# Kernel optimization log

Hardware: AMD Instinct MI355X
Metric: run time of the kernel (lower is better)

The kernel has to match this reference:

```python
import jax, jax.numpy as jnp
import numpy as np

E, H = 512, 256  # embed_dim, hidden_dim
B, SQ, SK = 2, 512, 512


def _linear_params(k, fin, fout):
    lim = 1.0 / np.sqrt(fin)
    kw, kb = jax.random.split(k)
    W = jax.random.uniform(kw, (fin, fout), minval=-lim, maxval=lim, dtype=jnp.float32)
    b = jax.random.uniform(kb, (fout,), minval=-lim, maxval=lim, dtype=jnp.float32)
    return W, b


def setup_inputs() -> dict:
    rng = jax.random.key(0)
    ks = jax.random.split(rng, 12)
    query = jax.random.normal(ks[0], (B, SQ, E), dtype=jnp.float32)
    key = jax.random.normal(ks[1], (B, SK, E), dtype=jnp.float32)
    Wqe, bqe = _linear_params(ks[2], E, H)
    Wke, bke = _linear_params(ks[3], E, H)
    W1, b1 = _linear_params(ks[4], 2 * H, H)  # importance_predictor layer 0
    W2, b2 = _linear_params(ks[5], H, H)      # layer 1
    W3, b3 = _linear_params(ks[6], H, H)      # layer 2
    Wf, bf = _linear_params(ks[7], H, 1)      # final importance logit
    Wv1, bv1 = _linear_params(ks[8], 2 * H, H)  # variance_estimator layer 0
    Wv2, bv2 = _linear_params(ks[9], H, 1)      # variance_estimator final
    return {"query": query, "key": key,
            "Wqe": Wqe, "bqe": bqe, "Wke": Wke, "bke": bke,
            "W1": W1, "b1": b1, "W2": W2, "b2": b2, "W3": W3, "b3": b3,
            "Wf": Wf, "bf": bf, "Wv1": Wv1, "bv1": bv1, "Wv2": Wv2, "bv2": bv2}


def reference(query, key, Wqe, bqe, Wke, bke, W1, b1, W2, b2, W3, b3, Wf, bf, Wv1, bv1, Wv2, bv2):
    # Encoders (dropout is identity at eval)
    qf = jax.nn.relu(jnp.einsum('bqe,eh->bqh', query, Wqe) + bqe)  # [B,Sq,H]
    kf = jax.nn.relu(jnp.einsum('bke,eh->bkh', key, Wke) + bke)    # [B,Sk,H]

    # First Linear(2H,H) on cat([q,k]) == q@W1[:H] + k@W1[H:]; broadcast over pairs
    qp = jnp.einsum('bqh,hd->bqd', qf, W1[:H])
    kp = jnp.einsum('bkh,hd->bkd', kf, W1[H:])
    h = jax.nn.relu(qp[:, :, None, :] + kp[:, None, :, :] + b1)  # [B,Sq,Sk,H]
    h = jax.nn.relu(jnp.einsum('bqkh,hd->bqkd', h, W2) + b2)
    h = jax.nn.relu(jnp.einsum('bqkh,hd->bqkd', h, W3) + b3)
    importance_logits = (jnp.einsum('bqkh,ho->bqko', h, Wf) + bf)[..., 0]  # [B,Sq,Sk]

    # Variance head: Linear(2H,H) split the same way, ReLU, Linear, Softplus
    vq = jnp.einsum('bqh,hd->bqd', qf, Wv1[:H])
    vk = jnp.einsum('bkh,hd->bkd', kf, Wv1[H:])
    v = jax.nn.relu(vq[:, :, None, :] + vk[:, None, :, :] + bv1)  # [B,Sq,Sk,H]
    estimated_variance = jax.nn.softplus((jnp.einsum('bqkh,ho->bqko', v, Wv2) + bv2)[..., 0])
    return importance_logits, estimated_variance
```

## Files before the change

kernel.cpp:

```cpp
#include <hip/hip_runtime.h>
#include <hip/hip_bf16.h>
#include <cstdint>
#include <cstddef>
#include <cstring>

#define HDIM 256
#define EDIM 512
#define NB   2
#define NSQ  512
#define NSK  512

typedef _Float16 f16x8 __attribute__((ext_vector_type(8)));
typedef _Float16 h2    __attribute__((ext_vector_type(2)));
typedef __fp16   fp16v2 __attribute__((ext_vector_type(2)));
typedef float    f32x4 __attribute__((ext_vector_type(4)));
typedef unsigned short u16x8 __attribute__((ext_vector_type(8)));

#define OFF_W2F  0u
#define OFF_W3F  65536u
#define OFF_WQEF 131072u
#define OFF_WKEF 262144u
#define OFF_WCQ  393216u
#define OFF_WCK  524288u
#define OFF_WV2H 655360u
#define F16_WS_END_BYTES 1312768u

union U8 { f16x8 v; h2 h[4]; };

__device__ __forceinline__ ushort2 f2h2(float x, float y) {
  fp16v2 r = __builtin_amdgcn_cvt_pkrtz(x, y);
  ushort2 u;
  __builtin_memcpy(&u, &r, 4);
  return u;
}
__device__ __forceinline__ float relu_(float x) { return x > 0.f ? x : 0.f; }
__device__ __forceinline__ float softplus_(float x) {
  return fmaxf(x, 0.f) + log1pf(expf(-fabsf(x)));
}

__global__ __launch_bounds__(64) void shuffle_weights(
    const float* __restrict__ Wqe, const float* __restrict__ Wke,
    const float* __restrict__ W1,  const float* __restrict__ Wv1,
    const float* __restrict__ W2,  const float* __restrict__ W3,
    const float* __restrict__ Wv2,
    unsigned short* __restrict__ wsb)
{
  const int bx = blockIdx.x;
  const int lane = threadIdx.x;
  if (bx == 1280) {
    float a = Wv2[lane * 4 + 0], b = Wv2[lane * 4 + 1];
    float c = Wv2[lane * 4 + 2], d = Wv2[lane * 4 + 3];
    ushort2 lo = f2h2(a, b), hi = f2h2(c, d);
    ushort4 o; o.x = lo.x; o.y = lo.y; o.z = hi.x; o.w = hi.y;
    *(ushort4*)&wsb[OFF_WV2H + lane * 4] = o;
    return;
  }
  const float* src; unsigned short* dst; int S; int idx;
  if      (bx <  128) { src = W2;          dst = wsb + OFF_W2F;           S = 8;  idx = bx;        }
  else if (bx <  256) { src = W3;          dst = wsb + OFF_W3F;           S = 8;  idx = bx - 128;  }
  else if (bx <  512) { src = Wqe;         dst = wsb + OFF_WQEF;          S = 16; idx = bx - 256;  }
  else if (bx <  768) { src = Wke;         dst = wsb + OFF_WKEF;          S = 16; idx = bx - 512;  }
  else if (bx <  896) { src = W1;          dst = wsb + OFF_WCQ;           S = 8;  idx = bx - 768;  }
  else if (bx < 1024) { src = Wv1;         dst = wsb + OFF_WCQ + 65536u;  S = 8;  idx = bx - 896;  }
  else if (bx < 1152) { src = W1 + 65536;  dst = wsb + OFF_WCK;           S = 8;  idx = bx - 1024; }
  else                { src = Wv1 + 65536; dst = wsb + OFF_WCK + 65536u;  S = 8;  idx = bx - 1152; }
  const int t = idx / S, s = idx % S;
  const int n  = t * 16 + (lane & 15);
  const int k0 = s * 32 + ((lane >> 4) << 3);
  unsigned short* o = dst + ((size_t)(t * S + s) * 64 + lane) * 8;
  #pragma unroll
  for (int j = 0; j < 8; j += 2) {
    ushort2 pp = f2h2(src[(size_t)(k0 + j) * 256 + n], src[(size_t)(k0 + j + 1) * 256 + n]);
    *(ushort2*)&o[j] = pp;
  }
}

__global__ __launch_bounds__(256) void encoder_kernel(
    const float* __restrict__ query, const float* __restrict__ key,
    const float* __restrict__ bqe,   const float* __restrict__ bke,
    const float* __restrict__ b1,    const float* __restrict__ bv1,
    const unsigned short* __restrict__ WqeF, const unsigned short* __restrict__ WkeF,
    const unsigned short* __restrict__ WcqF, const unsigned short* __restrict__ WckF,
    _Float16* __restrict__ Pq, _Float16* __restrict__ Pk)
{
  __shared__ unsigned short sX[32 * 520];
  __shared__ unsigned short sF[32 * 264];
  __shared__ float sBe[256];
  __shared__ float sBc[512];

  const int bx   = blockIdx.x;
  const int side = bx >> 5;
  const int rt   = bx & 31;
  const int t    = threadIdx.x;

  const float* Xsrc = side ? key : query;
  const unsigned short* WeF = side ? WkeF : WqeF;
  const unsigned short* WcF = side ? WckF : WcqF;
  _Float16* P = side ? Pk : Pq;

  {
    const int m = t >> 3, ch = t & 7;
    const int c0 = ch * 64;
    const float* xr = Xsrc + (size_t)(rt * 32 + m) * EDIM;
    #pragma unroll
    for (int cc = 0; cc < 64; cc += 4) {
      const int c = c0 + cc;
      float4 xv = *(const float4*)(xr + c);
      ushort2 lo = f2h2(xv.x, xv.y);
      ushort2 hi = f2h2(xv.z, xv.w);
      ushort4 xb; xb.x = lo.x; xb.y = lo.y; xb.z = hi.x; xb.w = hi.y;
      *(ushort4*)&sX[m * 520 + c] = xb;
    }
    sBe[t]       = side ? bke[t] : bqe[t];
    sBc[t]       = side ? 0.f : b1[t];
    sBc[256 + t] = side ? 0.f : bv1[t];
  }
  __syncthreads();

  const int wave = t >> 6, lane = t & 63;
  const int l15 = lane & 15, q4 = lane >> 4;

  f32x4 acc1[4][2];
  #pragma unroll
  for (int ft = 0; ft < 4; ++ft)
    #pragma unroll
    for (int pt = 0; pt < 2; ++pt)
      acc1[ft][pt] = (f32x4){0.f, 0.f, 0.f, 0.f};

  for (int s = 0; s < 16; ++s) {
    f16x8 af[4], bfr[2];
    #pragma unroll
    for (int ft = 0; ft < 4; ++ft) {
      const int tg = wave * 4 + ft;
      af[ft] = *(const f16x8*)(WeF + ((size_t)(tg * 16 + s) * 64 + lane) * 8);
    }
    #pragma unroll
    for (int pt = 0; pt < 2; ++pt)
      bfr[pt] = *(const f16x8*)&sX[(pt * 16 + l15) * 520 + s * 32 + q4 * 8];
    #pragma unroll
    for (int ft = 0; ft < 4; ++ft)
      #pragma unroll
      for (int pt = 0; pt < 2; ++pt)
        acc1[ft][pt] = __builtin_amdgcn_mfma_f32_16x16x32_f16(af[ft], bfr[pt], acc1[ft][pt], 0, 0, 0);
  }

  #pragma unroll
  for (int ft = 0; ft < 4; ++ft) {
    const int tg = wave * 4 + ft;
    const int n0 = tg * 16 + q4 * 4;
    float4 b4 = *(const float4*)&sBe[n0];
    #pragma unroll
    for (int pt = 0; pt < 2; ++pt) {
      const int mr = pt * 16 + l15;
      f32x4 a = acc1[ft][pt];
      ushort2 lo = f2h2(relu_(a[0] + b4.x), relu_(a[1] + b4.y));
      ushort2 hi = f2h2(relu_(a[2] + b4.z), relu_(a[3] + b4.w));
      ushort4 h; h.x = lo.x; h.y = lo.y; h.z = hi.x; h.w = hi.y;
      *(ushort4*)&sF[mr * 264 + n0] = h;
    }
  }
  __syncthreads();

  f32x4 acc2[8][2];
  #pragma unroll
  for (int ft = 0; ft < 8; ++ft)
    #pragma unroll
    for (int pt = 0; pt < 2; ++pt)
      acc2[ft][pt] = (f32x4){0.f, 0.f, 0.f, 0.f};

  for (int s = 0; s < 8; ++s) {
    f16x8 af[8], bfr[2];
    #pragma unroll
    for (int ft = 0; ft < 8; ++ft) {
      const int tg = wave * 8 + ft;
      af[ft] = *(const f16x8*)(WcF + ((size_t)(tg * 8 + s) * 64 + lane) * 8);
    }
    #pragma unroll
    for (int pt = 0; pt < 2; ++pt)
      bfr[pt] = *(const f16x8*)&sF[(pt * 16 + l15) * 264 + s * 32 + q4 * 8];
    #pragma unroll
    for (int ft = 0; ft < 8; ++ft)
      #pragma unroll
      for (int pt = 0; pt < 2; ++pt)
        acc2[ft][pt] = __builtin_amdgcn_mfma_f32_16x16x32_f16(af[ft], bfr[pt], acc2[ft][pt], 0, 0, 0);
  }

  #pragma unroll
  for (int ft = 0; ft < 8; ++ft) {
    const int tg = wave * 8 + ft;
    const int n0 = tg * 16 + q4 * 4;
    float4 bc = *(const float4*)&sBc[n0];
    #pragma unroll
    for (int pt = 0; pt < 2; ++pt) {
      const int mr = pt * 16 + l15;
      const int row = rt * 32 + mr;
      f32x4 a = acc2[ft][pt];
      ushort2 lo = f2h2(a[0] + bc.x, a[1] + bc.y);
      ushort2 hi = f2h2(a[2] + bc.z, a[3] + bc.w);
      ushort4 o; o.x = lo.x; o.y = lo.y; o.z = hi.x; o.w = hi.y;
      *(ushort4*)((unsigned short*)P + (size_t)row * 512 + n0) = o;
    }
  }
}

__global__ __launch_bounds__(512, 4) void pair_kernel(
    const _Float16* __restrict__ Pq, const _Float16* __restrict__ Pk,
    const unsigned short* __restrict__ W2F, const unsigned short* __restrict__ W3F,
    const float* __restrict__ b2, const float* __restrict__ b3,
    const float* __restrict__ Wf, const float* __restrict__ bfp,
    const unsigned short* __restrict__ Wv2H, const float* __restrict__ bv2p,
    float* __restrict__ out)
{
  __shared__ __align__(16) unsigned char smem[35840];
  unsigned short* sXH = (unsigned short*)smem;
  float* sB2   = (float*)(smem + 32768);
  float* sB3   = (float*)(smem + 33792);
  float* sWf   = (float*)(smem + 34816);
  float* sRed  = (float*)(smem + 32768);

  const int kt = blockIdx.x, qy = blockIdx.y, bz = blockIdx.z;
  const int t = threadIdx.x;
  const _Float16* qpRow = Pq + (size_t)(bz * NSQ + qy) * 512;

  const int wave = t >> 6, lane = t & 63;
  const int l15 = lane & 15, q4 = lane >> 4;
  const int lsw = l15 & 7;

  const unsigned short* a2base = W2F + ((size_t)(wave * 2) * 8 * 64 + lane) * 8;
  const unsigned short* a3base = W3F + ((size_t)(wave * 2) * 8 * 64 + lane) * 8;

  f16x8 afd[2][2];
  afd[0][0] = *(const f16x8*)(a2base);
  afd[0][1] = *(const f16x8*)(a2base + 8 * 64 * 8);

  {
    const int m   = t >> 3;
    const int sub = t & 7;
    const _Float16* kpRow = Pk + (size_t)(bz * NSK + kt * 64 + m) * 512;
    const int msw = (m & 7);
    const f16x8 z8 = {0, 0, 0, 0, 0, 0, 0, 0};
    float vpart = 0.f;
    #pragma unroll
    for (int it = 0; it < 4; ++it) {
      const int c = it * 64 + sub * 8;
      f16x8 q8 = *(const f16x8*)(qpRow + c);
      f16x8 k8 = *(const f16x8*)(kpRow + c);
      f16x8 r  = __builtin_elementwise_max(q8 + k8, z8);
      const int chunk = (c >> 3) ^ msw;
      *(f16x8*)&sXH[m * 256 + chunk * 8] = r;
      f16x8 a8 = *(const f16x8*)(qpRow + 256 + c);
      f16x8 v8 = *(const f16x8*)(kpRow + 256 + c);
      U8 ar; ar.v = __builtin_elementwise_max(a8 + v8, z8);
      U8 w8; w8.v = *(const f16x8*)((const _Float16*)Wv2H + c);
      vpart = __builtin_amdgcn_fdot2(ar.h[0], w8.h[0], vpart, false);
      vpart = __builtin_amdgcn_fdot2(ar.h[1], w8.h[1], vpart, false);
      vpart = __builtin_amdgcn_fdot2(ar.h[2], w8.h[2], vpart, false);
      vpart = __builtin_amdgcn_fdot2(ar.h[3], w8.h[3], vpart, false);
    }
    vpart += __shfl_xor(vpart, 1, 64);
    vpart += __shfl_xor(vpart, 2, 64);
    vpart += __shfl_xor(vpart, 4, 64);
    if (sub == 0) {
      const size_t o = (size_t)(bz * NSQ + qy) * NSK + kt * 64 + m;
      out[(size_t)NB * NSQ * NSK + o] = softplus_(vpart + bv2p[0]);
    }
    if (t < 256) { sB2[t] = b2[t]; sB3[t] = b3[t]; sWf[t] = Wf[t]; }
  }
  __syncthreads();

  f32x4 acc[2][4];
  #pragma unroll
  for (int ft = 0; ft < 2; ++ft)
    #pragma unroll
    for (int pt = 0; pt < 4; ++pt)
      acc[ft][pt] = (f32x4){0.f, 0.f, 0.f, 0.f};

  #pragma unroll
  for (int s = 0; s < 8; ++s) {
    if (s < 7) {
      afd[(s + 1) & 1][0] = *(const f16x8*)(a2base + (size_t)(s + 1) * 512);
      afd[(s + 1) & 1][1] = *(const f16x8*)(a2base + 8 * 64 * 8 + (size_t)(s + 1) * 512);
    }
    f16x8 bfr[4];
    #pragma unroll
    for (int pt = 0; pt < 4; ++pt) {
      const int chunk = ((s << 2) + q4) ^ lsw;
      bfr[pt] = *(const f16x8*)&sXH[(pt * 16 + l15) * 256 + chunk * 8];
    }
    #pragma unroll
    for (int ft = 0; ft < 2; ++ft)
      #pragma unroll
      for (int pt = 0; pt < 4; ++pt)
        acc[ft][pt] = __builtin_amdgcn_mfma_f32_16x16x32_f16(afd[s & 1][ft], bfr[pt], acc[ft][pt], 0, 0, 0);
  }
  __syncthreads();

  afd[0][0] = *(const f16x8*)(a3base);
  afd[0][1] = *(const f16x8*)(a3base + 8 * 64 * 8);

  #pragma unroll
  for (int ft = 0; ft < 2; ++ft) {
    const int tg = wave * 2 + ft;
    const int n0 = tg * 16 + q4 * 4;
    float4 b4 = *(const float4*)&sB2[n0];
    const int chunkS = ((n0 >> 3) ^ lsw);
    #pragma unroll
    for (int pt = 0; pt < 4; ++pt) {
      const int mr = pt * 16 + l15;
      f32x4 a = acc[ft][pt];
      ushort2 lo = f2h2(relu_(a[0] + b4.x), relu_(a[1] + b4.y));
      ushort2 hi = f2h2(relu_(a[2] + b4.z), relu_(a[3] + b4.w));
      ushort4 h; h.x = lo.x; h.y = lo.y; h.z = hi.x; h.w = hi.y;
      *(ushort4*)&sXH[mr * 256 + chunkS * 8 + (n0 & 7)] = h;
    }
  }
  __syncthreads();

  f32x4 acc2[2][4];
  #pragma unroll
  for (int ft = 0; ft < 2; ++ft)
    #pragma unroll
    for (int pt = 0; pt < 4; ++pt)
      acc2[ft][pt] = (f32x4){0.f, 0.f, 0.f, 0.f};

  #pragma unroll
  for (int s = 0; s < 8; ++s) {
    if (s < 7) {
      afd[(s + 1) & 1][0] = *(const f16x8*)(a3base + (size_t)(s + 1) * 512);
      afd[(s + 1) & 1][1] = *(const f16x8*)(a3base + 8 * 64 * 8 + (size_t)(s + 1) * 512);
    }
    f16x8 bfr[4];
    #pragma unroll
    for (int pt = 0; pt < 4; ++pt) {
      const int chunk = ((s << 2) + q4) ^ lsw;
      bfr[pt] = *(const f16x8*)&sXH[(pt * 16 + l15) * 256 + chunk * 8];
    }
    #pragma unroll
    for (int ft = 0; ft < 2; ++ft)
      #pragma unroll
      for (int pt = 0; pt < 4; ++pt)
        acc2[ft][pt] = __builtin_amdgcn_mfma_f32_16x16x32_f16(afd[s & 1][ft], bfr[pt], acc2[ft][pt], 0, 0, 0);
  }

  float p[4] = {0.f, 0.f, 0.f, 0.f};
  #pragma unroll
  for (int ft = 0; ft < 2; ++ft) {
    const int tg = wave * 2 + ft;
    const int n0 = tg * 16 + q4 * 4;
    float4 b4 = *(const float4*)&sB3[n0];
    float4 w4 = *(const float4*)&sWf[n0];
    #pragma unroll
    for (int pt = 0; pt < 4; ++pt) {
      f32x4 a = acc2[ft][pt];
      p[pt] += relu_(a[0] + b4.x) * w4.x + relu_(a[1] + b4.y) * w4.y
             + relu_(a[2] + b4.z) * w4.z + relu_(a[3] + b4.w) * w4.w;
    }
  }
  __syncthreads();
  #pragma unroll
  for (int pt = 0; pt < 4; ++pt) {
    float v = p[pt];
    v += __shfl_xor(v, 16, 64);
    v += __shfl_xor(v, 32, 64);
    if (lane < 16) sRed[wave * 64 + pt * 16 + lane] = v;
  }
  __syncthreads();

  if (t < 64) {
    const size_t o = (size_t)(bz * NSQ + qy) * NSK + kt * 64 + t;
    float lg = bfp[0];
    #pragma unroll
    for (int w = 0; w < 8; ++w) lg += sRed[w * 64 + t];
    out[o] = lg;
  }
}

extern "C" void kernel_launch(void* const* d_in, const int* in_sizes, int n_in,
                              void* d_out, int out_size, void* d_ws, size_t ws_size,
                              hipStream_t stream)
{
  (void)in_sizes; (void)n_in; (void)out_size; (void)ws_size;
  const float* query = (const float*)d_in[0];
  const float* key   = (const float*)d_in[1];
  const float* Wqe   = (const float*)d_in[2];
  const float* bqe   = (const float*)d_in[3];
  const float* Wke   = (const float*)d_in[4];
  const float* bke   = (const float*)d_in[5];
  const float* W1    = (const float*)d_in[6];
  const float* b1    = (const float*)d_in[7];
  const float* W2    = (const float*)d_in[8];
  const float* b2    = (const float*)d_in[9];
  const float* W3    = (const float*)d_in[10];
  const float* b3    = (const float*)d_in[11];
  const float* Wf    = (const float*)d_in[12];
  const float* bf    = (const float*)d_in[13];
  const float* Wv1   = (const float*)d_in[14];
  const float* bv1   = (const float*)d_in[15];
  const float* Wv2   = (const float*)d_in[16];
  const float* bv2   = (const float*)d_in[17];

  unsigned short* wsb = (unsigned short*)d_ws;
  _Float16* Pq = (_Float16*)((char*)d_ws + F16_WS_END_BYTES);
  _Float16* Pk = Pq + (size_t)1024 * 512;
  float* out = (float*)d_out;

  shuffle_weights<<<1281, 64, 0, stream>>>(Wqe, Wke, W1, Wv1, W2, W3, Wv2, wsb);
  encoder_kernel<<<64, 256, 0, stream>>>(query, key, bqe, bke, b1, bv1,
      wsb + OFF_WQEF, wsb + OFF_WKEF, wsb + OFF_WCQ, wsb + OFF_WCK, Pq, Pk);
  pair_kernel<<<dim3(NSK / 64, NSQ, NB), 512, 0, stream>>>(Pq, Pk,
      wsb + OFF_W2F, wsb + OFF_W3F, b2, b3, Wf, bf, wsb + OFF_WV2H, bv2, out);
}
```

Measured before the change: 265.3 us.

## Coalesce weight shuffle via LDS, halve encoder tile, pad pair LDS rows

```diff
diff --git a/kernel.cpp b/kernel.cpp
--- a/kernel.cpp
+++ b/kernel.cpp
@@ -13,8 +13,7 @@
 typedef _Float16 f16x8 __attribute__((ext_vector_type(8)));
 typedef _Float16 h2    __attribute__((ext_vector_type(2)));
 typedef __fp16   fp16v2 __attribute__((ext_vector_type(2)));
-typedef float    f32x4 __attribute__((ext_vector_type(4)));
-typedef unsigned short u16x8 __attribute__((ext_vector_type(8)));
+typedef float    f32x4  __attribute__((ext_vector_type(4)));
 
 #define OFF_W2F  0u
 #define OFF_W3F  65536u
@@ -38,40 +37,60 @@
   return fmaxf(x, 0.f) + log1pf(expf(-fabsf(x)));
 }
 
-__global__ __launch_bounds__(64) void shuffle_weights(
+__global__ __launch_bounds__(256) void shuffle_weights(
     const float* __restrict__ Wqe, const float* __restrict__ Wke,
     const float* __restrict__ W1,  const float* __restrict__ Wv1,
     const float* __restrict__ W2,  const float* __restrict__ W3,
     const float* __restrict__ Wv2,
     unsigned short* __restrict__ wsb)
 {
+  __shared__ float sW[32 * 257];
   const int bx = blockIdx.x;
-  const int lane = threadIdx.x;
-  if (bx == 1280) {
-    float a = Wv2[lane * 4 + 0], b = Wv2[lane * 4 + 1];
-    float c = Wv2[lane * 4 + 2], d = Wv2[lane * 4 + 3];
-    ushort2 lo = f2h2(a, b), hi = f2h2(c, d);
-    ushort4 o; o.x = lo.x; o.y = lo.y; o.z = hi.x; o.w = hi.y;
-    *(ushort4*)&wsb[OFF_WV2H + lane * 4] = o;
+  const int t = threadIdx.x;
+  if (bx == 80) {
+    if (t < 64) {
+      float a = Wv2[t * 4 + 0], b = Wv2[t * 4 + 1];
+      float c = Wv2[t * 4 + 2], d = Wv2[t * 4 + 3];
+      ushort2 lo = f2h2(a, b), hi = f2h2(c, d);
+      ushort4 o; o.x = lo.x; o.y = lo.y; o.z = hi.x; o.w = hi.y;
+      *(ushort4*)&wsb[OFF_WV2H + t * 4] = o;
+    }
     return;
   }
-  const float* src; unsigned short* dst; int S; int idx;
-  if      (bx <  128) { src = W2;          dst = wsb + OFF_W2F;           S = 8;  idx = bx;        }
-  else if (bx <  256) { src = W3;          dst = wsb + OFF_W3F;           S = 8;  idx = bx - 128;  }
-  else if (bx <  512) { src = Wqe;         dst = wsb + OFF_WQEF;          S = 16; idx = bx - 256;  }
-  else if (bx <  768) { src = Wke;         dst = wsb + OFF_WKEF;          S = 16; idx = bx - 512;  }
-  else if (bx <  896) { src = W1;          dst = wsb + OFF_WCQ;           S = 8;  idx = bx - 768;  }
-  else if (bx < 1024) { src = Wv1;         dst = wsb + OFF_WCQ + 65536u;  S = 8;  idx = bx - 896;  }
-  else if (bx < 1152) { src = W1 + 65536;  dst = wsb + OFF_WCK;           S = 8;  idx = bx - 1024; }
-  else                { src = Wv1 + 65536; dst = wsb + OFF_WCK + 65536u;  S = 8;  idx = bx - 1152; }
-  const int t = idx / S, s = idx % S;
-  const int n  = t * 16 + (lane & 15);
-  const int k0 = s * 32 + ((lane >> 4) << 3);
-  unsigned short* o = dst + ((size_t)(t * S + s) * 64 + lane) * 8;
-  #pragma unroll
-  for (int j = 0; j < 8; j += 2) {
-    ushort2 pp = f2h2(src[(size_t)(k0 + j) * 256 + n], src[(size_t)(k0 + j + 1) * 256 + n]);
-    *(ushort2*)&o[j] = pp;
+  const float* src; unsigned short* dst; int s; int S;
+  if      (bx <  8) { src = W2;          dst = wsb + OFF_W2F;           s = bx;      S = 8;  }
+  else if (bx < 16) { src = W3;          dst = wsb + OFF_W3F;           s = bx - 8;  S = 8;  }
+  else if (bx < 32) { src = Wqe;         dst = wsb + OFF_WQEF;          s = bx - 16; S = 16; }
+  else if (bx < 48) { src = Wke;         dst = wsb + OFF_WKEF;          s = bx - 32; S = 16; }
+  else if (bx < 56) { src = W1;          dst = wsb + OFF_WCQ;           s = bx - 48; S = 8;  }
+  else if (bx < 64) { src = Wv1;         dst = wsb + OFF_WCQ + 65536u;  s = bx - 56; S = 8;  }
+  else if (bx < 72) { src = W1 + 65536;  dst = wsb + OFF_WCK;           s = bx - 64; S = 8;  }
+  else              { src = Wv1 + 65536; dst = wsb + OFF_WCK + 65536u;  s = bx - 72; S = 8;  }
+
+  const int kbase = s * 32;
+  #pragma unroll
+  for (int it = 0; it < 8; ++it) {
+    const int f4 = it * 256 + t;
+    const int row = f4 >> 6, c4 = (f4 & 63) * 4;
+    float4 v = *(const float4*)(src + (size_t)(kbase + row) * 256 + c4);
+    sW[row * 257 + c4 + 0] = v.x; sW[row * 257 + c4 + 1] = v.y;
+    sW[row * 257 + c4 + 2] = v.z; sW[row * 257 + c4 + 3] = v.w;
+  }
+  __syncthreads();
+
+  const int wave = t >> 6, lane = t & 63;
+  const int n_in = lane & 15, k0 = (lane >> 4) * 8;
+  for (int tt = wave * 4; tt < wave * 4 + 4; ++tt) {
+    const int n = tt * 16 + n_in;
+    float x[8];
+    #pragma unroll
+    for (int j = 0; j < 8; ++j) x[j] = sW[(k0 + j) * 257 + n];
+    ushort2 p0 = f2h2(x[0], x[1]), p1 = f2h2(x[2], x[3]);
+    ushort2 p2 = f2h2(x[4], x[5]), p3 = f2h2(x[6], x[7]);
+    ushort4 lo; lo.x = p0.x; lo.y = p0.y; lo.z = p1.x; lo.w = p1.y;
+    ushort4 hi; hi.x = p2.x; hi.y = p2.y; hi.z = p3.x; hi.w = p3.y;
+    unsigned short* o = dst + ((size_t)(tt * S + s) * 64 + lane) * 8;
+    *(ushort4*)&o[0] = lo; *(ushort4*)&o[4] = hi;
   }
 }
 
@@ -83,14 +102,14 @@
     const unsigned short* __restrict__ WcqF, const unsigned short* __restrict__ WckF,
     _Float16* __restrict__ Pq, _Float16* __restrict__ Pk)
 {
-  __shared__ unsigned short sX[32 * 520];
-  __shared__ unsigned short sF[32 * 264];
+  __shared__ unsigned short sX[16 * 520];
+  __shared__ unsigned short sF[16 * 264];
   __shared__ float sBe[256];
   __shared__ float sBc[512];
 
   const int bx   = blockIdx.x;
-  const int side = bx >> 5;
-  const int rt   = bx & 31;
+  const int side = bx >> 6;
+  const int rt   = bx & 63;
   const int t    = threadIdx.x;
 
   const float* Xsrc = side ? key : query;
@@ -99,17 +118,19 @@
   _Float16* P = side ? Pk : Pq;
 
   {
-    const int m = t >> 3, ch = t & 7;
-    const int c0 = ch * 64;
-    const float* xr = Xsrc + (size_t)(rt * 32 + m) * EDIM;
-    #pragma unroll
-    for (int cc = 0; cc < 64; cc += 4) {
-      const int c = c0 + cc;
-      float4 xv = *(const float4*)(xr + c);
-      ushort2 lo = f2h2(xv.x, xv.y);
-      ushort2 hi = f2h2(xv.z, xv.w);
-      ushort4 xb; xb.x = lo.x; xb.y = lo.y; xb.z = hi.x; xb.w = hi.y;
-      *(ushort4*)&sX[m * 520 + c] = xb;
+    const int m = t >> 4, ch = t & 15;
+    const float* xr = Xsrc + (size_t)(rt * 16 + m) * EDIM;
+    #pragma unroll
+    for (int j = 0; j < 4; ++j) {
+      const int c = ch * 32 + j * 8;
+      float4 v0 = *(const float4*)(xr + c);
+      float4 v1 = *(const float4*)(xr + c + 4);
+      ushort2 p0 = f2h2(v0.x, v0.y), p1 = f2h2(v0.z, v0.w);
+      ushort2 p2 = f2h2(v1.x, v1.y), p3 = f2h2(v1.z, v1.w);
+      ushort4 lo; lo.x = p0.x; lo.y = p0.y; lo.z = p1.x; lo.w = p1.y;
+      ushort4 hi; hi.x = p2.x; hi.y = p2.y; hi.z = p3.x; hi.w = p3.y;
+      *(ushort4*)&sX[m * 520 + c] = lo;
+      *(ushort4*)&sX[m * 520 + c + 4] = hi;
     }
     sBe[t]       = side ? bke[t] : bqe[t];
     sBc[t]       = side ? 0.f : b1[t];
@@ -120,28 +141,21 @@
   const int wave = t >> 6, lane = t & 63;
   const int l15 = lane & 15, q4 = lane >> 4;
 
-  f32x4 acc1[4][2];
-  #pragma unroll
-  for (int ft = 0; ft < 4; ++ft)
-    #pragma unroll
-    for (int pt = 0; pt < 2; ++pt)
-      acc1[ft][pt] = (f32x4){0.f, 0.f, 0.f, 0.f};
+  f32x4 acc1[4];
+  #pragma unroll
+  for (int ft = 0; ft < 4; ++ft) acc1[ft] = (f32x4){0.f, 0.f, 0.f, 0.f};
 
   for (int s = 0; s < 16; ++s) {
-    f16x8 af[4], bfr[2];
+    f16x8 af[4], bfr;
     #pragma unroll
     for (int ft = 0; ft < 4; ++ft) {
       const int tg = wave * 4 + ft;
       af[ft] = *(const f16x8*)(WeF + ((size_t)(tg * 16 + s) * 64 + lane) * 8);
     }
-    #pragma unroll
-    for (int pt = 0; pt < 2; ++pt)
-      bfr[pt] = *(const f16x8*)&sX[(pt * 16 + l15) * 520 + s * 32 + q4 * 8];
+    bfr = *(const f16x8*)&sX[l15 * 520 + s * 32 + q4 * 8];
     #pragma unroll
     for (int ft = 0; ft < 4; ++ft)
-      #pragma unroll
-      for (int pt = 0; pt < 2; ++pt)
-        acc1[ft][pt] = __builtin_amdgcn_mfma_f32_16x16x32_f16(af[ft], bfr[pt], acc1[ft][pt], 0, 0, 0);
+      acc1[ft] = __builtin_amdgcn_mfma_f32_16x16x32_f16(af[ft], bfr, acc1[ft], 0, 0, 0);
   }
 
   #pragma unroll
@@ -149,40 +163,29 @@
     const int tg = wave * 4 + ft;
     const int n0 = tg * 16 + q4 * 4;
     float4 b4 = *(const float4*)&sBe[n0];
-    #pragma unroll
-    for (int pt = 0; pt < 2; ++pt) {
-      const int mr = pt * 16 + l15;
-      f32x4 a = acc1[ft][pt];
-      ushort2 lo = f2h2(relu_(a[0] + b4.x), relu_(a[1] + b4.y));
-      ushort2 hi = f2h2(relu_(a[2] + b4.z), relu_(a[3] + b4.w));
-      ushort4 h; h.x = lo.x; h.y = lo.y; h.z = hi.x; h.w = hi.y;
-      *(ushort4*)&sF[mr * 264 + n0] = h;
-    }
-  }
-  __syncthreads();
-
-  f32x4 acc2[8][2];
-  #pragma unroll
-  for (int ft = 0; ft < 8; ++ft)
-    #pragma unroll
-    for (int pt = 0; pt < 2; ++pt)
-      acc2[ft][pt] = (f32x4){0.f, 0.f, 0.f, 0.f};
+    f32x4 a = acc1[ft];
+    ushort2 lo = f2h2(relu_(a[0] + b4.x), relu_(a[1] + b4.y));
+    ushort2 hi = f2h2(relu_(a[2] + b4.z), relu_(a[3] + b4.w));
+    ushort4 h; h.x = lo.x; h.y = lo.y; h.z = hi.x; h.w = hi.y;
+    *(ushort4*)&sF[l15 * 264 + n0] = h;
+  }
+  __syncthreads();
+
+  f32x4 acc2[8];
+  #pragma unroll
+  for (int ft = 0; ft < 8; ++ft) acc2[ft] = (f32x4){0.f, 0.f, 0.f, 0.f};
 
   for (int s = 0; s < 8; ++s) {
-    f16x8 af[8], bfr[2];
+    f16x8 af[8], bfr;
     #pragma unroll
     for (int ft = 0; ft < 8; ++ft) {
       const int tg = wave * 8 + ft;
       af[ft] = *(const f16x8*)(WcF + ((size_t)(tg * 8 + s) * 64 + lane) * 8);
     }
-    #pragma unroll
-    for (int pt = 0; pt < 2; ++pt)
-      bfr[pt] = *(const f16x8*)&sF[(pt * 16 + l15) * 264 + s * 32 + q4 * 8];
+    bfr = *(const f16x8*)&sF[l15 * 264 + s * 32 + q4 * 8];
     #pragma unroll
     for (int ft = 0; ft < 8; ++ft)
-      #pragma unroll
-      for (int pt = 0; pt < 2; ++pt)
-        acc2[ft][pt] = __builtin_amdgcn_mfma_f32_16x16x32_f16(af[ft], bfr[pt], acc2[ft][pt], 0, 0, 0);
+      acc2[ft] = __builtin_amdgcn_mfma_f32_16x16x32_f16(af[ft], bfr, acc2[ft], 0, 0, 0);
   }
 
   #pragma unroll
@@ -190,16 +193,12 @@
     const int tg = wave * 8 + ft;
     const int n0 = tg * 16 + q4 * 4;
     float4 bc = *(const float4*)&sBc[n0];
-    #pragma unroll
-    for (int pt = 0; pt < 2; ++pt) {
-      const int mr = pt * 16 + l15;
-      const int row = rt * 32 + mr;
-      f32x4 a = acc2[ft][pt];
-      ushort2 lo = f2h2(a[0] + bc.x, a[1] + bc.y);
-      ushort2 hi = f2h2(a[2] + bc.z, a[3] + bc.w);
-      ushort4 o; o.x = lo.x; o.y = lo.y; o.z = hi.x; o.w = hi.y;
-      *(ushort4*)((unsigned short*)P + (size_t)row * 512 + n0) = o;
-    }
+    const int row = rt * 16 + l15;
+    f32x4 a = acc2[ft];
+    ushort2 lo = f2h2(a[0] + bc.x, a[1] + bc.y);
+    ushort2 hi = f2h2(a[2] + bc.z, a[3] + bc.w);
+    ushort4 o; o.x = lo.x; o.y = lo.y; o.z = hi.x; o.w = hi.y;
+    *(ushort4*)((unsigned short*)P + (size_t)row * 512 + n0) = o;
   }
 }
 
@@ -211,12 +210,12 @@
     const unsigned short* __restrict__ Wv2H, const float* __restrict__ bv2p,
     float* __restrict__ out)
 {
-  __shared__ __align__(16) unsigned char smem[35840];
+  __shared__ __align__(16) unsigned char smem[36864];
   unsigned short* sXH = (unsigned short*)smem;
-  float* sB2   = (float*)(smem + 32768);
-  float* sB3   = (float*)(smem + 33792);
-  float* sWf   = (float*)(smem + 34816);
-  float* sRed  = (float*)(smem + 32768);
+  float* sB2  = (float*)(smem + 33792);
+  float* sB3  = (float*)(smem + 34816);
+  float* sWf  = (float*)(smem + 35840);
+  float* sRed = (float*)(smem + 33792);
 
   const int kt = blockIdx.x, qy = blockIdx.y, bz = blockIdx.z;
   const int t = threadIdx.x;
@@ -224,7 +223,6 @@
 
   const int wave = t >> 6, lane = t & 63;
   const int l15 = lane & 15, q4 = lane >> 4;
-  const int lsw = l15 & 7;
 
   const unsigned short* a2base = W2F + ((size_t)(wave * 2) * 8 * 64 + lane) * 8;
   const unsigned short* a3base = W3F + ((size_t)(wave * 2) * 8 * 64 + lane) * 8;
@@ -237,7 +235,6 @@
     const int m   = t >> 3;
     const int sub = t & 7;
     const _Float16* kpRow = Pk + (size_t)(bz * NSK + kt * 64 + m) * 512;
-    const int msw = (m & 7);
     const f16x8 z8 = {0, 0, 0, 0, 0, 0, 0, 0};
     float vpart = 0.f;
     #pragma unroll
@@ -246,8 +243,7 @@
       f16x8 q8 = *(const f16x8*)(qpRow + c);
       f16x8 k8 = *(const f16x8*)(kpRow + c);
       f16x8 r  = __builtin_elementwise_max(q8 + k8, z8);
-      const int chunk = (c >> 3) ^ msw;
-      *(f16x8*)&sXH[m * 256 + chunk * 8] = r;
+      *(f16x8*)&sXH[m * 264 + c] = r;
       f16x8 a8 = *(const f16x8*)(qpRow + 256 + c);
       f16x8 v8 = *(const f16x8*)(kpRow + 256 + c);
       U8 ar; ar.v = __builtin_elementwise_max(a8 + v8, z8);
@@ -283,10 +279,8 @@
     }
     f16x8 bfr[4];
     #pragma unroll
-    for (int pt = 0; pt < 4; ++pt) {
-      const int chunk = ((s << 2) + q4) ^ lsw;
-      bfr[pt] = *(const f16x8*)&sXH[(pt * 16 + l15) * 256 + chunk * 8];
-    }
+    for (int pt = 0; pt < 4; ++pt)
+      bfr[pt] = *(const f16x8*)&sXH[(pt * 16 + l15) * 264 + s * 32 + q4 * 8];
     #pragma unroll
     for (int ft = 0; ft < 2; ++ft)
       #pragma unroll
@@ -303,7 +297,6 @@
     const int tg = wave * 2 + ft;
     const int n0 = tg * 16 + q4 * 4;
     float4 b4 = *(const float4*)&sB2[n0];
-    const int chunkS = ((n0 >> 3) ^ lsw);
     #pragma unroll
     for (int pt = 0; pt < 4; ++pt) {
       const int mr = pt * 16 + l15;
@@ -311,7 +304,7 @@
       ushort2 lo = f2h2(relu_(a[0] + b4.x), relu_(a[1] + b4.y));
       ushort2 hi = f2h2(relu_(a[2] + b4.z), relu_(a[3] + b4.w));
       ushort4 h; h.x = lo.x; h.y = lo.y; h.z = hi.x; h.w = hi.y;
-      *(ushort4*)&sXH[mr * 256 + chunkS * 8 + (n0 & 7)] = h;
+      *(ushort4*)&sXH[mr * 264 + n0] = h;
     }
   }
   __syncthreads();
@@ -331,10 +324,8 @@
     }
     f16x8 bfr[4];
     #pragma unroll
-    for (int pt = 0; pt < 4; ++pt) {
-      const int chunk = ((s << 2) + q4) ^ lsw;
-      bfr[pt] = *(const f16x8*)&sXH[(pt * 16 + l15) * 256 + chunk * 8];
-    }
+    for (int pt = 0; pt < 4; ++pt)
+      bfr[pt] = *(const f16x8*)&sXH[(pt * 16 + l15) * 264 + s * 32 + q4 * 8];
     #pragma unroll
     for (int ft = 0; ft < 2; ++ft)
       #pragma unroll
@@ -404,8 +395,8 @@
   _Float16* Pk = Pq + (size_t)1024 * 512;
   float* out = (float*)d_out;
 
-  shuffle_weights<<<1281, 64, 0, stream>>>(Wqe, Wke, W1, Wv1, W2, W3, Wv2, wsb);
-  encoder_kernel<<<64, 256, 0, stream>>>(query, key, bqe, bke, b1, bv1,
+  shuffle_weights<<<81, 256, 0, stream>>>(Wqe, Wke, W1, Wv1, W2, W3, Wv2, wsb);
+  encoder_kernel<<<128, 256, 0, stream>>>(query, key, bqe, bke, b1, bv1,
       wsb + OFF_WQEF, wsb + OFF_WKEF, wsb + OFF_WCQ, wsb + OFF_WCK, Pq, Pk);
   pair_kernel<<<dim3(NSK / 64, NSQ, NB), 512, 0, stream>>>(Pq, Pk,
       wsb + OFF_W2F, wsb + OFF_W3F, b2, b3, Wf, bf, wsb + OFF_WV2H, bv2, out);
```

Result: slower. 275.1 us (+3.7%).
